# Optimization experiments

Measured on AMD Instinct MI355X. Metric: run time of the kernel, lower is better.

## Reference

```python
import jax, jax.numpy as jnp
import numpy as np

B, C, T, H, W = 4, 512, 16, 32, 32
NUM_HEADS = 8
GROUPS = 32
MAX_REL = 64
EPS = 1e-6
HEAD_DIM = C // NUM_HEADS


def setup_inputs() -> dict:
    key = jax.random.key(0)
    ks = jax.random.split(key, 9)
    inp = {
        "x": jax.random.normal(ks[0], (B, C, T, H, W), dtype=jnp.float32),
        "gamma": 1.0 + 0.02 * jax.random.normal(ks[1], (C,), dtype=jnp.float32),
        "beta": 0.02 * jax.random.normal(ks[2], (C,), dtype=jnp.float32),
        "w_qkv": jax.random.normal(ks[3], (3 * C, C), dtype=jnp.float32) / np.sqrt(C),
        "b_qkv": 0.02 * jax.random.normal(ks[4], (3 * C,), dtype=jnp.float32),
        "rp_k": jax.random.normal(ks[5], (2 * MAX_REL + 1, HEAD_DIM), dtype=jnp.float32) * 0.02,
        "rp_v": jax.random.normal(ks[6], (2 * MAX_REL + 1, HEAD_DIM), dtype=jnp.float32) * 0.02,
        "w_proj": jax.random.normal(ks[7], (C, C), dtype=jnp.float32) / np.sqrt(C),
        "b_proj": 0.02 * jax.random.normal(ks[8], (C,), dtype=jnp.float32),
    }
    return inp


def reference(x, gamma, beta, w_qkv, b_qkv, rp_k, rp_v, w_proj, b_proj):
    b, c, t, h, w = x.shape
    # 'b c t h w -> (b h w) c t'
    seq = x.transpose(0, 3, 4, 1, 2).reshape(b * h * w, c, t)
    N = seq.shape[0]
    # GroupNorm over (channels_per_group, t)
    g = seq.reshape(N, GROUPS, (c // GROUPS) * t)
    mean = g.mean(axis=-1, keepdims=True)
    var = g.var(axis=-1, keepdims=True)
    g = (g - mean) * jax.lax.rsqrt(var + EPS)
    normed = g.reshape(N, c, t) * gamma[None, :, None] + beta[None, :, None]
    # qkv 1x1 conv == matmul over channel dim
    qkv = jnp.einsum('oc,nct->not', w_qkv, normed) + b_qkv[None, :, None]
    q, k, v = jnp.split(qkv, 3, axis=1)  # each [N, C, T]
    ch = c // NUM_HEADS
    scale = float(ch) ** -0.25
    qh = (q * scale).reshape(N * NUM_HEADS, ch, t)
    kh = (k * scale).reshape(N * NUM_HEADS, ch, t)
    vh = v.reshape(N * NUM_HEADS, ch, t)
    # content scores
    weight = jnp.einsum('bct,bcs->bts', qh, kh)  # [B*, t, s]
    # relative position embeddings [t, t, ch]
    dist = jnp.clip(jnp.arange(t)[None, :] - jnp.arange(t)[:, None], -MAX_REL, MAX_REL) + MAX_REL
    k_emb = rp_k[dist]
    v_emb = rp_v[dist]
    # faithful to original: weight2 is 'bst' and added to 'bts' weight directly
    weight = weight + jnp.einsum('bct,tsc->bst', qh, k_emb)
    weight = jax.nn.softmax(weight.astype(jnp.float32), axis=-1).astype(weight.dtype)
    a = jnp.einsum('bts,bcs->bct', weight, vh)
    a = a + jnp.einsum('bts,tsc->btc', weight, v_emb).transpose(0, 2, 1)
    out = a.reshape(N, c, t)
    out = jnp.einsum('oc,nct->not', w_proj, out) + b_proj[None, :, None]
    # '(b h w) c t -> b c t h w'
    out = out.reshape(b, h, w, c, t).transpose(0, 3, 4, 1, 2)
    return x + out
```

## Files before the change

kernel.cpp:

```cpp
#include <hip/hip_runtime.h>

typedef __attribute__((ext_vector_type(8))) short bf16x8;
typedef __attribute__((ext_vector_type(4))) float f32x4;

#define MFMA16(a, b, c) __builtin_amdgcn_mfma_f32_16x16x32_bf16((a), (b), (c), 0, 0, 0)

__device__ inline ushort f2bf(float f) {
    union { float f; unsigned u; } a; a.f = f;
    unsigned r = a.u + 0x7fffu + ((a.u >> 16) & 1u);
    return (ushort)(r >> 16);
}
__device__ inline float bf2f(ushort h) {
    union { unsigned u; float f; } a; a.u = ((unsigned)h) << 16;
    return a.f;
}
__device__ inline void gload_lds16(const void* g, void* l) {
    __builtin_amdgcn_global_load_lds((const __attribute__((address_space(1))) unsigned*)g,
                                     (__attribute__((address_space(3))) unsigned*)l, 16, 0, 0);
}

__global__ __launch_bounds__(256) void k_convw(
    const float* __restrict__ wq, const float* __restrict__ wp,
    ushort* __restrict__ dst) {
    size_t e = ((size_t)blockIdx.x * 256 + threadIdx.x) * 4;
    float4 v;
    if (e < 786432) v = *(const float4*)(wq + e);
    else            v = *(const float4*)(wp + (e - 786432));
    ushort4 o;
    o.x = f2bf(v.x); o.y = f2bf(v.y); o.z = f2bf(v.z); o.w = f2bf(v.w);
    *(ushort4*)(dst + e) = o;
}

__global__ __launch_bounds__(256) void k_groupnorm(
    const float* __restrict__ x, const float* __restrict__ gamma,
    const float* __restrict__ beta, ushort* __restrict__ A) {
    __shared__ float red_s[4][64], red_q[4][64];
    __shared__ float sm_mean[64], sm_rstd[64];
    int tid = threadIdx.x;
    int nb = blockIdx.x, g = blockIdx.y;
    int n_base = nb * 64;
    int b_idx = n_base >> 10;
    int hw_base = n_base & 1023;
    int n_loc = tid & 63, w = tid >> 6;

    const float* xb = x + (size_t)(b_idx * 512 + g * 16) * 16 * 1024 + hw_base + n_loc;
    float s = 0.f, sq = 0.f;
    #pragma unroll 4
    for (int i = 0; i < 64; ++i) {
        int k = w + 4 * i;
        float v = xb[(size_t)k * 1024];
        s += v; sq += v * v;
    }
    red_s[w][n_loc] = s; red_q[w][n_loc] = sq;
    __syncthreads();
    if (tid < 64) {
        float ts = red_s[0][tid] + red_s[1][tid] + red_s[2][tid] + red_s[3][tid];
        float tq = red_q[0][tid] + red_q[1][tid] + red_q[2][tid] + red_q[3][tid];
        float mean = ts * (1.f / 256.f);
        float var = tq * (1.f / 256.f) - mean * mean;
        sm_mean[tid] = mean;
        sm_rstd[tid] = rsqrtf(var + 1e-6f);
    }
    __syncthreads();

    int nl = tid & 63;
    float mean = sm_mean[nl], rstd = sm_rstd[nl];
    #pragma unroll
    for (int it = 0; it < 4; ++it) {
        int t2 = it * 4 + (tid >> 6);
        const float* xs = x + ((size_t)(b_idx * 512 + g * 16) * 16 + t2) * 1024 + hw_base + nl;
        union { ushort u[16]; uint4 v[2]; } pk;
        #pragma unroll
        for (int cc = 0; cc < 16; ++cc) {
            float v = xs[(size_t)cc * 16 * 1024];
            float y = (v - mean) * rstd * gamma[g * 16 + cc] + beta[g * 16 + cc];
            pk.u[cc] = f2bf(y);
        }
        ushort* dst = A + ((size_t)(n_base + nl) * 16 + t2) * 512 + g * 16;
        ((uint4*)dst)[0] = pk.v[0];
        ((uint4*)dst)[1] = pk.v[1];
    }
}

__global__ __launch_bounds__(256) void k_gemm(
    const ushort* __restrict__ Abf, const ushort* __restrict__ Wbf,
    const float* __restrict__ bias, ushort* __restrict__ Cbf, int Nn) {
    __shared__ ushort aT[128 * 32];
    __shared__ ushort bT[128 * 32];
    int tid = threadIdx.x, lane = tid & 63, wv = tid >> 6;
    int wm = wv >> 1, wn = wv & 1;
    int l15 = lane & 15, g4 = lane >> 4;
    int n0 = blockIdx.x * 128;
    size_t m0 = (size_t)blockIdx.y * 128;
    f32x4 acc[4][4];
    #pragma unroll
    for (int i = 0; i < 4; ++i)
        #pragma unroll
        for (int j = 0; j < 4; ++j) acc[i][j] = (f32x4){0.f, 0.f, 0.f, 0.f};

    int rowA = lane >> 2;
    int kcol = (lane & 3) * 8;
    const ushort* Ab = Abf + (m0 + rowA) * 512 + kcol;
    const ushort* Bb = Wbf + (size_t)(n0 + rowA) * 512 + kcol;

    for (int kk = 0; kk < 512; kk += 32) {
        if (kk) __syncthreads();
        #pragma unroll
        for (int r = 0; r < 2; ++r) {
            int rb = (r * 4 + wv) * 16;
            gload_lds16(Ab + (size_t)rb * 512 + kk, &aT[rb * 32]);
            gload_lds16(Bb + (size_t)rb * 512 + kk, &bT[rb * 32]);
        }
        __syncthreads();
        bf16x8 af[4], bfr[4];
        #pragma unroll
        for (int i = 0; i < 4; ++i) {
            af[i]  = *(const bf16x8*)(&aT[(wm * 64 + i * 16 + l15) * 32 + g4 * 8]);
            bfr[i] = *(const bf16x8*)(&bT[(wn * 64 + i * 16 + l15) * 32 + g4 * 8]);
        }
        #pragma unroll
        for (int i = 0; i < 4; ++i)
            #pragma unroll
            for (int j = 0; j < 4; ++j)
                acc[i][j] = MFMA16(af[i], bfr[j], acc[i][j]);
    }
    #pragma unroll
    for (int j = 0; j < 4; ++j) {
        int col = n0 + wn * 64 + j * 16 + l15;
        float bi = bias[col];
        #pragma unroll
        for (int i = 0; i < 4; ++i) {
            size_t rowb = m0 + wm * 64 + i * 16 + g4 * 4;
            #pragma unroll
            for (int r = 0; r < 4; ++r)
                Cbf[(rowb + r) * (size_t)Nn + col] = f2bf(acc[i][j][r] + bi);
        }
    }
}

__global__ __launch_bounds__(128) void k_attn(
    const ushort* __restrict__ C1, const float* __restrict__ rp_k,
    const float* __restrict__ rp_v, ushort* __restrict__ O) {
    __shared__ ushort rpk_s[32 * 64];
    __shared__ ushort rpvT_s[64 * 32];
    __shared__ ushort q_s[2][16 * 64];
    __shared__ ushort k_s[2][16 * 64];
    __shared__ ushort v2_s[2][64 * 32];
    __shared__ ushort wbf_s[2][16 * 32];
    __shared__ ushort w2_s[2][16 * 32];
    __shared__ float  pa_s[2][32 * 17];

    int tid = threadIdx.x, lane = tid & 63, wv = tid >> 6;
    for (int q = 0; q < 16; ++q) {
        int e = tid * 16 + q;
        int d = e >> 6, c = e & 63;
        rpk_s[e] = (d < 31) ? f2bf(rp_k[(size_t)(49 + d) * 64 + c]) : (ushort)0;
        int c2 = e >> 5, d2 = e & 31;
        rpvT_s[e] = (d2 < 31) ? f2bf(rp_v[(size_t)(49 + d2) * 64 + c2]) : (ushort)0;
    }
    __syncthreads();

    int bh = blockIdx.x * 2 + wv;
    int n = bh >> 3, head = bh & 7;
    const ushort* base = C1 + (size_t)n * 16 * 1536 + head * 64;
    ushort* qp = q_s[wv]; ushort* kp = k_s[wv]; ushort* vp = v2_s[wv];
    int t8 = lane >> 3, c8 = (lane & 7) * 8;
    #pragma unroll
    for (int p = 0; p < 2; ++p) {
        int t = p * 8 + t8;
        const ushort* rb = base + (size_t)t * 1536;
        *(uint4*)(&qp[t * 64 + c8]) = *(const uint4*)(rb + c8);
        *(uint4*)(&kp[t * 64 + c8]) = *(const uint4*)(rb + 512 + c8);
        uint4 vvv = *(const uint4*)(rb + 1024 + c8);
        const ushort* vu = (const ushort*)&vvv;
        #pragma unroll
        for (int qq = 0; qq < 8; ++qq) vp[(c8 + qq) * 32 + t] = vu[qq];
    }
    { uint4 z = {0, 0, 0, 0};
      *(uint4*)(&vp[lane * 32 + 16]) = z;
      *(uint4*)(&vp[lane * 32 + 24]) = z; }

    int l15 = lane & 15, g4 = lane >> 4;
    bf16x8 qf0 = *(const bf16x8*)(&qp[l15 * 64 + g4 * 8]);
    bf16x8 qf1 = *(const bf16x8*)(&qp[l15 * 64 + 32 + g4 * 8]);
    bf16x8 kf0 = *(const bf16x8*)(&kp[l15 * 64 + g4 * 8]);
    bf16x8 kf1 = *(const bf16x8*)(&kp[l15 * 64 + 32 + g4 * 8]);
    f32x4 zero = {0.f, 0.f, 0.f, 0.f};
    f32x4 wc = MFMA16(qf0, kf0, zero);
    wc = MFMA16(qf1, kf1, wc);
    f32x4 P0, P1;
    {
        bf16x8 rk;
        rk = *(const bf16x8*)(&rpk_s[l15 * 64 + g4 * 8]);             P0 = MFMA16(rk, qf0, zero);
        rk = *(const bf16x8*)(&rpk_s[l15 * 64 + 32 + g4 * 8]);        P0 = MFMA16(rk, qf1, P0);
        rk = *(const bf16x8*)(&rpk_s[(16 + l15) * 64 + g4 * 8]);      P1 = MFMA16(rk, qf0, zero);
        rk = *(const bf16x8*)(&rpk_s[(16 + l15) * 64 + 32 + g4 * 8]); P1 = MFMA16(rk, qf1, P1);
    }
    float* pa = pa_s[wv];
    #pragma unroll
    for (int r = 0; r < 4; ++r) {
        pa[(g4 * 4 + r) * 17 + l15] = P0[r];
        pa[(16 + g4 * 4 + r) * 17 + l15] = P1[r];
    }
    ushort* wb = wbf_s[wv];
    #pragma unroll
    for (int r = 0; r < 4; ++r) {
        int i = g4 * 4 + r;
        float sc = 0.125f * wc[r] + 0.35355339059327373f * pa[(i - l15 + 15) * 17 + l15];
        float mx = sc;
        mx = fmaxf(mx, __shfl_xor(mx, 1));
        mx = fmaxf(mx, __shfl_xor(mx, 2));
        mx = fmaxf(mx, __shfl_xor(mx, 4));
        mx = fmaxf(mx, __shfl_xor(mx, 8));
        float e = __expf(sc - mx);
        float sm = e;
        sm += __shfl_xor(sm, 1); sm += __shfl_xor(sm, 2);
        sm += __shfl_xor(sm, 4); sm += __shfl_xor(sm, 8);
        float p = e / sm;
        wb[i * 32 + l15] = f2bf(p);
        wb[i * 32 + 16 + l15] = 0;
    }
    ushort* w2 = w2_s[wv];
    #pragma unroll
    for (int q = 0; q < 8; ++q) {
        int e = lane * 8 + q;
        int i = e >> 5, d = e & 31;
        int j = i + d - 15;
        ushort val = 0;
        if (d < 31 && j >= 0 && j < 16) val = wb[i * 32 + j];
        w2[e] = val;
    }
    bf16x8 wfr = *(const bf16x8*)(&wb[l15 * 32 + g4 * 8]);
    bf16x8 w2f = *(const bf16x8*)(&w2[l15 * 32 + g4 * 8]);
    ushort* ob = O + (size_t)n * 16 * 512 + head * 64;
    #pragma unroll
    for (int cj = 0; cj < 4; ++cj) {
        bf16x8 vf  = *(const bf16x8*)(&vp[(cj * 16 + l15) * 32 + g4 * 8]);
        bf16x8 rvf = *(const bf16x8*)(&rpvT_s[(cj * 16 + l15) * 32 + g4 * 8]);
        f32x4 av = MFMA16(wfr, vf, zero);
        av = MFMA16(w2f, rvf, av);
        #pragma unroll
        for (int r = 0; r < 4; ++r)
            ob[(size_t)(g4 * 4 + r) * 512 + cj * 16 + l15] = f2bf(av[r]);
    }
}

__global__ __launch_bounds__(256) void k_out(
    const ushort* __restrict__ C2, const float* __restrict__ x,
    float* __restrict__ out) {
    __shared__ ushort tile[64 * 74];
    int tid = threadIdx.x;
    int idx = blockIdx.x;
    int hw0 = (idx & 15) * 64;
    int c0 = ((idx >> 4) & 7) * 64;
    int t = (idx >> 7) & 15;
    int b = idx >> 11;
    #pragma unroll
    for (int p = 0; p < 2; ++p) {
        int hw_l = p * 32 + (tid >> 3);
        int c8 = (tid & 7) * 8;
        size_t m = (size_t)(b * 1024 + hw0 + hw_l) * 16 + t;
        union { uint4 v; ushort u[8]; } un;
        un.v = *(const uint4*)(C2 + m * 512 + c0 + c8);
        #pragma unroll
        for (int q = 0; q < 8; ++q) tile[hw_l * 74 + c8 + q] = un.u[q];
    }
    __syncthreads();
    #pragma unroll
    for (int it = 0; it < 16; ++it) {
        int flat = it * 256 + tid;
        int c_l = flat >> 6, hw_l = flat & 63;
        float v = bf2f(tile[hw_l * 74 + c_l]);
        size_t oi = ((size_t)(b * 512 + c0 + c_l) * 16 + t) * 1024 + hw0 + hw_l;
        out[oi] = x[oi] + v;
    }
}

extern "C" void kernel_launch(void* const* d_in, const int* in_sizes, int n_in,
                              void* d_out, int out_size, void* d_ws, size_t ws_size,
                              hipStream_t stream) {
    const float* x      = (const float*)d_in[0];
    const float* gamma  = (const float*)d_in[1];
    const float* beta   = (const float*)d_in[2];
    const float* w_qkv  = (const float*)d_in[3];
    const float* b_qkv  = (const float*)d_in[4];
    const float* rp_k   = (const float*)d_in[5];
    const float* rp_v   = (const float*)d_in[6];
    const float* w_proj = (const float*)d_in[7];
    const float* b_proj = (const float*)d_in[8];
    float* out = (float*)d_out;

    ushort* A  = (ushort*)d_ws;
    ushort* C1 = A + (size_t)32 * 1024 * 1024;
    ushort* C2 = C1;
    ushort* Wq = (ushort*)d_out;
    ushort* Wp = Wq + 1536 * 512;

    k_convw<<<dim3(1024), dim3(256), 0, stream>>>(w_qkv, w_proj, Wq);
    k_groupnorm<<<dim3(64, 32), dim3(256), 0, stream>>>(x, gamma, beta, A);
    k_gemm<<<dim3(12, 512), dim3(256), 0, stream>>>(A, Wq, b_qkv, C1, 1536);
    k_attn<<<dim3(16384), dim3(128), 0, stream>>>(C1, rp_k, rp_v, A);
    k_gemm<<<dim3(4, 512), dim3(256), 0, stream>>>(A, Wp, b_proj, C2, 512);
    k_out<<<dim3(8192), dim3(256), 0, stream>>>(C2, x, out);
}
```

Baseline: 689.8 us.

## Double-buffer GEMM LDS, remap blocks per XCD, precompute rel-pos tables, rework output transpose

The GEMM now double-buffers its LDS tiles so the next K-slice loads while MFMAs run on the current one. Work-groups are remapped so each XCD handles a contiguous band of M rows, which should improve L2 reuse. The relative-position tables are converted to bf16 once in the weight-convert kernel instead of in every attention block, and the V tile in LDS gets padding to reduce bank conflicts. The output kernel uses a new tile shape with an XOR-swizzled LDS transpose. The cost is twice the GEMM LDS footprint, which may lower occupancy.

```diff
diff --git a/kernel.cpp b/kernel.cpp
--- a/kernel.cpp
+++ b/kernel.cpp
@@ -21,14 +21,29 @@
 
 __global__ __launch_bounds__(256) void k_convw(
     const float* __restrict__ wq, const float* __restrict__ wp,
+    const float* __restrict__ rp_k, const float* __restrict__ rp_v,
     ushort* __restrict__ dst) {
-    size_t e = ((size_t)blockIdx.x * 256 + threadIdx.x) * 4;
-    float4 v;
-    if (e < 786432) v = *(const float4*)(wq + e);
-    else            v = *(const float4*)(wp + (e - 786432));
-    ushort4 o;
-    o.x = f2bf(v.x); o.y = f2bf(v.y); o.z = f2bf(v.z); o.w = f2bf(v.w);
-    *(ushort4*)(dst + e) = o;
+    int tid = threadIdx.x;
+    if (blockIdx.x < 1024) {
+        size_t e = ((size_t)blockIdx.x * 256 + tid) * 4;
+        float4 v;
+        if (e < 786432) v = *(const float4*)(wq + e);
+        else            v = *(const float4*)(wp + (e - 786432));
+        ushort4 o;
+        o.x = f2bf(v.x); o.y = f2bf(v.y); o.z = f2bf(v.z); o.w = f2bf(v.w);
+        *(ushort4*)(dst + e) = o;
+    } else {
+        ushort* rpk_g  = dst + 1048576;
+        ushort* rpvT_g = rpk_g + 2048;
+        #pragma unroll
+        for (int q = 0; q < 8; ++q) {
+            int e = tid * 8 + q;
+            int d = e >> 6, c = e & 63;
+            rpk_g[e] = (d < 31) ? f2bf(rp_k[(size_t)(49 + d) * 64 + c]) : (ushort)0;
+            int c2 = e >> 5, d2 = e & 31;
+            rpvT_g[e] = (d2 < 31) ? f2bf(rp_v[(size_t)(49 + d2) * 64 + c2]) : (ushort)0;
+        }
+    }
 }
 
 __global__ __launch_bounds__(256) void k_groupnorm(
@@ -84,14 +99,20 @@
 
 __global__ __launch_bounds__(256) void k_gemm(
     const ushort* __restrict__ Abf, const ushort* __restrict__ Wbf,
-    const float* __restrict__ bias, ushort* __restrict__ Cbf, int Nn) {
-    __shared__ ushort aT[128 * 32];
-    __shared__ ushort bT[128 * 32];
+    const float* __restrict__ bias, ushort* __restrict__ Cbf,
+    int Nn, int nb, int mpx) {
+    __shared__ ushort aT[2][128 * 32];
+    __shared__ ushort bT[2][128 * 32];
     int tid = threadIdx.x, lane = tid & 63, wv = tid >> 6;
     int wm = wv >> 1, wn = wv & 1;
     int l15 = lane & 15, g4 = lane >> 4;
-    int n0 = blockIdx.x * 128;
-    size_t m0 = (size_t)blockIdx.y * 128;
+    int wg = blockIdx.x;
+    int xcd = wg & 7, idx = wg >> 3;
+    int mp = xcd * mpx + idx / nb;
+    int np = idx % nb;
+    size_t m0 = (size_t)mp * 128;
+    int n0 = np * 128;
+
     f32x4 acc[4][4];
     #pragma unroll
     for (int i = 0; i < 4; ++i)
@@ -103,27 +124,35 @@
     const ushort* Ab = Abf + (m0 + rowA) * 512 + kcol;
     const ushort* Bb = Wbf + (size_t)(n0 + rowA) * 512 + kcol;
 
-    for (int kk = 0; kk < 512; kk += 32) {
-        if (kk) __syncthreads();
-        #pragma unroll
-        for (int r = 0; r < 2; ++r) {
-            int rb = (r * 4 + wv) * 16;
-            gload_lds16(Ab + (size_t)rb * 512 + kk, &aT[rb * 32]);
-            gload_lds16(Bb + (size_t)rb * 512 + kk, &bT[rb * 32]);
-        }
-        __syncthreads();
+#define STAGE(buf, kk) { \
+    _Pragma("unroll") \
+    for (int r = 0; r < 2; ++r) { \
+        int rb = (r * 4 + wv) * 16; \
+        gload_lds16(Ab + (size_t)rb * 512 + (kk), &aT[buf][rb * 32]); \
+        gload_lds16(Bb + (size_t)rb * 512 + (kk), &bT[buf][rb * 32]); \
+    } }
+
+    STAGE(0, 0)
+    __syncthreads();
+    int cur = 0;
+    for (int t = 0; t < 16; ++t) {
+        if (t < 15) STAGE(cur ^ 1, (t + 1) * 32)
         bf16x8 af[4], bfr[4];
         #pragma unroll
         for (int i = 0; i < 4; ++i) {
-            af[i]  = *(const bf16x8*)(&aT[(wm * 64 + i * 16 + l15) * 32 + g4 * 8]);
-            bfr[i] = *(const bf16x8*)(&bT[(wn * 64 + i * 16 + l15) * 32 + g4 * 8]);
+            af[i]  = *(const bf16x8*)(&aT[cur][(wm * 64 + i * 16 + l15) * 32 + g4 * 8]);
+            bfr[i] = *(const bf16x8*)(&bT[cur][(wn * 64 + i * 16 + l15) * 32 + g4 * 8]);
         }
         #pragma unroll
         for (int i = 0; i < 4; ++i)
             #pragma unroll
             for (int j = 0; j < 4; ++j)
                 acc[i][j] = MFMA16(af[i], bfr[j], acc[i][j]);
-    }
+        __syncthreads();
+        cur ^= 1;
+    }
+#undef STAGE
+
     #pragma unroll
     for (int j = 0; j < 4; ++j) {
         int col = n0 + wn * 64 + j * 16 + l15;
@@ -139,25 +168,22 @@
 }
 
 __global__ __launch_bounds__(128) void k_attn(
-    const ushort* __restrict__ C1, const float* __restrict__ rp_k,
-    const float* __restrict__ rp_v, ushort* __restrict__ O) {
+    const ushort* __restrict__ C1, const ushort* __restrict__ rpk_g,
+    const ushort* __restrict__ rpvT_g, ushort* __restrict__ O) {
     __shared__ ushort rpk_s[32 * 64];
     __shared__ ushort rpvT_s[64 * 32];
     __shared__ ushort q_s[2][16 * 64];
     __shared__ ushort k_s[2][16 * 64];
-    __shared__ ushort v2_s[2][64 * 32];
+    __shared__ ushort v2_s[2][64 * 40];
     __shared__ ushort wbf_s[2][16 * 32];
     __shared__ ushort w2_s[2][16 * 32];
     __shared__ float  pa_s[2][32 * 17];
 
     int tid = threadIdx.x, lane = tid & 63, wv = tid >> 6;
-    for (int q = 0; q < 16; ++q) {
-        int e = tid * 16 + q;
-        int d = e >> 6, c = e & 63;
-        rpk_s[e] = (d < 31) ? f2bf(rp_k[(size_t)(49 + d) * 64 + c]) : (ushort)0;
-        int c2 = e >> 5, d2 = e & 31;
-        rpvT_s[e] = (d2 < 31) ? f2bf(rp_v[(size_t)(49 + d2) * 64 + c2]) : (ushort)0;
-    }
+    *(uint4*)(&rpk_s[tid * 16])      = *(const uint4*)(rpk_g + tid * 16);
+    *(uint4*)(&rpk_s[tid * 16 + 8])  = *(const uint4*)(rpk_g + tid * 16 + 8);
+    *(uint4*)(&rpvT_s[tid * 16])     = *(const uint4*)(rpvT_g + tid * 16);
+    *(uint4*)(&rpvT_s[tid * 16 + 8]) = *(const uint4*)(rpvT_g + tid * 16 + 8);
     __syncthreads();
 
     int bh = blockIdx.x * 2 + wv;
@@ -174,11 +200,11 @@
         uint4 vvv = *(const uint4*)(rb + 1024 + c8);
         const ushort* vu = (const ushort*)&vvv;
         #pragma unroll
-        for (int qq = 0; qq < 8; ++qq) vp[(c8 + qq) * 32 + t] = vu[qq];
+        for (int qq = 0; qq < 8; ++qq) vp[(c8 + qq) * 40 + t] = vu[qq];
     }
     { uint4 z = {0, 0, 0, 0};
-      *(uint4*)(&vp[lane * 32 + 16]) = z;
-      *(uint4*)(&vp[lane * 32 + 24]) = z; }
+      *(uint4*)(&vp[lane * 40 + 16]) = z;
+      *(uint4*)(&vp[lane * 40 + 24]) = z; }
 
     int l15 = lane & 15, g4 = lane >> 4;
     bf16x8 qf0 = *(const bf16x8*)(&qp[l15 * 64 + g4 * 8]);
@@ -235,7 +261,7 @@
     ushort* ob = O + (size_t)n * 16 * 512 + head * 64;
     #pragma unroll
     for (int cj = 0; cj < 4; ++cj) {
-        bf16x8 vf  = *(const bf16x8*)(&vp[(cj * 16 + l15) * 32 + g4 * 8]);
+        bf16x8 vf  = *(const bf16x8*)(&vp[(cj * 16 + l15) * 40 + g4 * 8]);
         bf16x8 rvf = *(const bf16x8*)(&rpvT_s[(cj * 16 + l15) * 32 + g4 * 8]);
         f32x4 av = MFMA16(wfr, vf, zero);
         av = MFMA16(w2f, rvf, av);
@@ -248,31 +274,36 @@
 __global__ __launch_bounds__(256) void k_out(
     const ushort* __restrict__ C2, const float* __restrict__ x,
     float* __restrict__ out) {
-    __shared__ ushort tile[64 * 74];
+    __shared__ uint tw[32 * 16 * 8];
     int tid = threadIdx.x;
     int idx = blockIdx.x;
-    int hw0 = (idx & 15) * 64;
-    int c0 = ((idx >> 4) & 7) * 64;
-    int t = (idx >> 7) & 15;
-    int b = idx >> 11;
-    #pragma unroll
-    for (int p = 0; p < 2; ++p) {
-        int hw_l = p * 32 + (tid >> 3);
-        int c8 = (tid & 7) * 8;
-        size_t m = (size_t)(b * 1024 + hw0 + hw_l) * 16 + t;
-        union { uint4 v; ushort u[8]; } un;
-        un.v = *(const uint4*)(C2 + m * 512 + c0 + c8);
-        #pragma unroll
-        for (int q = 0; q < 8; ++q) tile[hw_l * 74 + c8 + q] = un.u[q];
-    }
-    __syncthreads();
-    #pragma unroll
-    for (int it = 0; it < 16; ++it) {
+    int cb = idx & 31, hwb = (idx >> 5) & 31, b = idx >> 10;
+    int c0 = cb * 16, hw0 = hwb * 32;
+    size_t mbase = ((size_t)(b * 1024 + hw0)) * 16;
+    #pragma unroll
+    for (int it = 0; it < 4; ++it) {
         int flat = it * 256 + tid;
-        int c_l = flat >> 6, hw_l = flat & 63;
-        float v = bf2f(tile[hw_l * 74 + c_l]);
-        size_t oi = ((size_t)(b * 512 + c0 + c_l) * 16 + t) * 1024 + hw0 + hw_l;
-        out[oi] = x[oi] + v;
+        int row = flat >> 1, cc8 = (flat & 1) * 8;
+        int hw = row >> 4, t = row & 15;
+        uint4 v = *(const uint4*)(C2 + (mbase + row) * 512 + c0 + cc8);
+        uint wbase = hw * 128 + t * 8;
+        uint s = hw & 7;
+        int j0 = cc8 >> 1;
+        tw[wbase + ((j0 + 0) ^ s)] = v.x;
+        tw[wbase + ((j0 + 1) ^ s)] = v.y;
+        tw[wbase + ((j0 + 2) ^ s)] = v.z;
+        tw[wbase + ((j0 + 3) ^ s)] = v.w;
+    }
+    __syncthreads();
+    #pragma unroll
+    for (int it = 0; it < 32; ++it) {
+        int flat = it * 256 + tid;
+        int hw = flat & 31, ct = flat >> 5;
+        int t = ct & 15, c = ct >> 4;
+        uint word = tw[hw * 128 + t * 8 + (((unsigned)c >> 1) ^ (unsigned)(hw & 7))];
+        ushort u = (c & 1) ? (ushort)(word >> 16) : (ushort)(word & 0xffff);
+        size_t oi = ((size_t)(b * 512 + c0 + c) * 16 + t) * 1024 + hw0 + hw;
+        out[oi] = x[oi] + bf2f(u);
     }
 }
 
@@ -294,12 +325,14 @@
     ushort* C1 = A + (size_t)32 * 1024 * 1024;
     ushort* C2 = C1;
     ushort* Wq = (ushort*)d_out;
-    ushort* Wp = Wq + 1536 * 512;
-
-    k_convw<<<dim3(1024), dim3(256), 0, stream>>>(w_qkv, w_proj, Wq);
+    ushort* Wp = Wq + 786432;
+    ushort* rpk_g  = Wq + 1048576;
+    ushort* rpvT_g = rpk_g + 2048;
+
+    k_convw<<<dim3(1025), dim3(256), 0, stream>>>(w_qkv, w_proj, rp_k, rp_v, Wq);
     k_groupnorm<<<dim3(64, 32), dim3(256), 0, stream>>>(x, gamma, beta, A);
-    k_gemm<<<dim3(12, 512), dim3(256), 0, stream>>>(A, Wq, b_qkv, C1, 1536);
-    k_attn<<<dim3(16384), dim3(128), 0, stream>>>(C1, rp_k, rp_v, A);
-    k_gemm<<<dim3(4, 512), dim3(256), 0, stream>>>(A, Wp, b_proj, C2, 512);
-    k_out<<<dim3(8192), dim3(256), 0, stream>>>(C2, x, out);
-}
+    k_gemm<<<dim3(6144), dim3(256), 0, stream>>>(A, Wq, b_qkv, C1, 1536, 12, 64);
+    k_attn<<<dim3(16384), dim3(128), 0, stream>>>(C1, rpk_g, rpvT_g, A);
+    k_gemm<<<dim3(2048), dim3(256), 0, stream>>>(A, Wp, b_proj, C2, 512, 4, 64);
+    k_out<<<dim3(4096), dim3(256), 0, stream>>>(C2, x, out);
+}
```

Result: faster. 647.3 us (-6.2%).
